# Kernel tuning notes

Measured on AMD Instinct MI355X. Metric: run time of the kernel, lower is better.

The kernel has to match this reference:

```python
import jax, jax.numpy as jnp
import numpy as np

NUM_HEADS = 8


def setup_inputs() -> dict:
    key = jax.random.key(0)
    ks = jax.random.split(key, 9)
    B, S, E = 16, 2048, 768
    s = 0.02
    return {
        "features": jax.random.normal(ks[0], (B, S, E), jnp.float32),
        "in_proj_w": jax.random.normal(ks[1], (3 * E, E), jnp.float32) * s,
        "in_proj_b": jnp.zeros((3 * E,), jnp.float32),
        "out_proj_w": jax.random.normal(ks[2], (E, E), jnp.float32) * s,
        "out_proj_b": jnp.zeros((E,), jnp.float32),
        "w1": jax.random.normal(ks[3], (384, E), jnp.float32) * s,
        "b1": jnp.zeros((384,), jnp.float32),
        "w2": jax.random.normal(ks[4], (1, 384), jnp.float32) * s,
        "b2": jnp.zeros((1,), jnp.float32),
    }


def reference(features, in_proj_w, in_proj_b, out_proj_w, out_proj_b, w1, b1, w2, b2):
    # torch nn.MultiheadAttention default batch_first=False: dim 0 is the
    # attended sequence axis (length B here), dim 1 is the MHA batch (S).
    B, S, E = features.shape
    H = NUM_HEADS
    Dh = E // H
    qkv = features @ in_proj_w.T + in_proj_b          # (B, S, 3E)
    q, k, v = jnp.split(qkv, 3, axis=-1)
    q = q.reshape(B, S, H, Dh)
    k = k.reshape(B, S, H, Dh)
    v = v.reshape(B, S, H, Dh)
    scale = 1.0 / jnp.sqrt(jnp.asarray(Dh, features.dtype))
    # attention over axis-0 positions (l, m in 0..B-1), per (s, h)
    scores = jnp.einsum('lshd,mshd->shlm', q * scale, k)
    attn = jax.nn.softmax(scores, axis=-1)
    ctx = jnp.einsum('shlm,mshd->lshd', attn, v).reshape(B, S, E)
    attn_out = ctx @ out_proj_w.T + out_proj_b        # (B, S, E)
    # batched 2-layer MLP (replaces the Python per-row loop)
    h = jax.nn.relu(attn_out @ w1.T + b1)             # (B, S, 384)
    prob = h @ w2.T + b2                              # (B, S, 1)
    contacts = jnp.broadcast_to(prob, (B, S, S))      # contacts[:, i, :] = prob[:, i]
    return contacts
```

## Files before the change

### kernel.cpp

```cpp
#include <hip/hip_runtime.h>

typedef unsigned short u16;
typedef __attribute__((ext_vector_type(8))) __bf16 bf16x8;
typedef __attribute__((ext_vector_type(4))) float floatx4;

#define B_DIM  16
#define S_DIM  2048
#define E_DIM  768
#define HEADS  8
#define DHEAD  96
#define MROWS  32768
#define QKV_LD 2304
#define NT     12

#define GLDS(gp, lp) __builtin_amdgcn_global_load_lds( \
    (const __attribute__((address_space(1))) void*)(gp), \
    (__attribute__((address_space(3))) void*)(lp), 16, 0, 0)

__device__ __forceinline__ u16 f2b(float f) {
    unsigned u = __float_as_uint(f);
    u += 0x7fffu + ((u >> 16) & 1u);
    return (u16)(u >> 16);
}
__device__ __forceinline__ float blo(unsigned u) { return __uint_as_float(u << 16); }
__device__ __forceinline__ float bhi(unsigned u) { return __uint_as_float(u & 0xffff0000u); }

__device__ __forceinline__ void axpy8(float* acc, float p, uint4 v) {
    acc[0] += p * blo(v.x); acc[1] += p * bhi(v.x);
    acc[2] += p * blo(v.y); acc[3] += p * bhi(v.y);
    acc[4] += p * blo(v.z); acc[5] += p * bhi(v.z);
    acc[6] += p * blo(v.w); acc[7] += p * bhi(v.w);
}

__device__ __forceinline__ bf16x8 ldsw(const u16* half_base, int rowh, int cb) {
    return *(const bf16x8*)((const char*)half_base + rowh * 128 + (cb ^ ((rowh & 7) << 4)));
}

#define PB0 24576
#define PB1 26304
#define PB2 26592
#define PB3 27168
#define PB4 27552
__global__ __launch_bounds__(256) void prep(const float* __restrict__ features,
                                            const float* __restrict__ in_proj_w,
                                            const float* __restrict__ w1,
                                            const float* __restrict__ out_proj_w,
                                            const float* __restrict__ bo,
                                            const float* __restrict__ b1,
                                            u16* __restrict__ fbf, u16* __restrict__ wib,
                                            u16* __restrict__ w1b, u16* __restrict__ WoT,
                                            float* __restrict__ cbuf) {
    __shared__ float tsh[32][33];
    const int b = blockIdx.x, tid = threadIdx.x;
    if (b < PB2) {
        const float* src; u16* dst; long i;
        if (b < PB0)      { src = features;  dst = fbf; i = (long)b * 256 + tid; }
        else if (b < PB1) { src = in_proj_w; dst = wib; i = (long)(b - PB0) * 256 + tid; }
        else              { src = w1;        dst = w1b; i = (long)(b - PB1) * 256 + tid; }
        float4 f = ((const float4*)src)[i];
        ushort4 r;
        r.x = f2b(f.x); r.y = f2b(f.y); r.z = f2b(f.z); r.w = f2b(f.w);
        ((ushort4*)dst)[i] = r;
    } else if (b < PB3) {
        const int t = b - PB2;
        const int bxT = t % 24, byT = t / 24;
        const int tx = tid & 31, ty = tid >> 5;
        int x = bxT * 32 + tx;
        int y = byT * 32 + ty;
#pragma unroll
        for (int j = 0; j < 4; j++) tsh[ty + j * 8][tx] = out_proj_w[(long)(y + j * 8) * 768 + x];
        __syncthreads();
        x = byT * 32 + tx;
        y = bxT * 32 + ty;
#pragma unroll
        for (int j = 0; j < 4; j++) WoT[(long)(y + j * 8) * 768 + x] = f2b(tsh[tx][ty + j * 8]);
    } else {
        const int n = b - PB3;
        const float* row = w1 + (long)n * 768;
        float s = row[tid] * bo[tid] + row[tid + 256] * bo[tid + 256] + row[tid + 512] * bo[tid + 512];
#pragma unroll
        for (int off = 32; off > 0; off >>= 1) s += __shfl_xor(s, off);
        if ((tid & 63) == 0) tsh[0][tid >> 6] = s;
        __syncthreads();
        if (tid == 0) cbuf[n] = tsh[0][0] + tsh[0][1] + tsh[0][2] + tsh[0][3] + b1[n];
    }
}

__global__ __launch_bounds__(512, 2) void qkv256(const u16* __restrict__ A,
                                                 const u16* __restrict__ W,
                                                 const float* __restrict__ bias,
                                                 u16* __restrict__ Cout,
                                                 const u16* __restrict__ gA,
                                                 const u16* __restrict__ gW,
                                                 u16* __restrict__ gC) {
    __shared__ __align__(16) u16 lds[2 * 32768];
    const int tid = threadIdx.x;
    const int bx  = blockIdx.x;
    int bm, bn, ldc, Mvalid; const u16 *Aa, *Ww; const float* bs; u16* Co; bool perm;
    if (bx < 1152) {
        const int xcd = bx & 7;
        const int q   = bx >> 3;
        bn = q % 9;
        bm = (q / 9) * 8 + xcd;
        Aa = A; Ww = W; bs = bias; Co = Cout; ldc = QKV_LD; perm = true; Mvalid = 1 << 30;
    } else {
        const int g = bx - 1152;
        bn = g % 3; bm = g / 3;
        Aa = gA; Ww = gW; bs = nullptr; Co = gC; ldc = 768; perm = false; Mvalid = 384;
    }
    const int r0 = tid >> 3,        r1 = (tid + 512) >> 3;
    const int q0 = (tid & 7) ^ (r0 & 7), q1 = ((tid + 512) & 7) ^ (r1 & 7);
    const u16* pA0 = Aa + (long)(bm * 256 + r0) * 768 + q0 * 8;
    const u16* pA1 = Aa + (long)(bm * 256 + r1) * 768 + q1 * 8;
    const u16* pB0 = Ww + (long)(bn * 256 + r0) * 768 + q0 * 8;
    const u16* pB1 = Ww + (long)(bn * 256 + r1) * 768 + q1 * 8;
    u16* dA0 = lds + tid * 8;
    u16* dA1 = lds + 4096 + tid * 8;
    u16* dB0 = lds + 16384 + tid * 8;
    u16* dB1 = lds + 16384 + 4096 + tid * 8;

#define IS_A(h, p, t) do { \
    GLDS(pA0 + (h) * 98304 + (t) * 64, dA0 + (p) * 32768 + (h) * 8192); \
    GLDS(pA1 + (h) * 98304 + (t) * 64, dA1 + (p) * 32768 + (h) * 8192); } while (0)
#define IS_B(h, p, t) do { \
    GLDS(pB0 + (h) * 98304 + (t) * 64, dB0 + (p) * 32768 + (h) * 8192); \
    GLDS(pB1 + (h) * 98304 + (t) * 64, dB1 + (p) * 32768 + (h) * 8192); } while (0)
#define MFMA_PRE() do { \
    __builtin_amdgcn_s_barrier(); \
    asm volatile("s_waitcnt lgkmcnt(0)" ::: "memory"); \
    __builtin_amdgcn_sched_barrier(0); \
    __builtin_amdgcn_s_setprio(1); } while (0)
#define MFMA_POST() do { \
    __builtin_amdgcn_s_setprio(0); \
    __builtin_amdgcn_s_barrier(); } while (0)

    const int lane = tid & 63, wid = tid >> 6;
    const int wr = wid >> 2, wc = wid & 3;
    const int fr = lane & 15, fg = lane >> 4;
    const int fq2 = fg * 16;
    const int wb  = (wc & 1) * 64;
    const u16* bufA_base = lds + wr * 8192;
    const u16* bufB_base = lds + 16384 + (wc >> 1) * 8192;

    IS_A(0, 0, 0); IS_A(1, 0, 0); IS_B(0, 0, 0); IS_B(1, 0, 0);
    IS_A(0, 1, 1); IS_A(1, 1, 1);
    asm volatile("s_waitcnt vmcnt(4)" ::: "memory");
    __builtin_amdgcn_s_barrier();

    floatx4 acc[8][4] = {};
#pragma unroll 2
    for (int t = 0; t < NT; ++t) {
        const int p = t & 1, pn = p ^ 1;
        const u16* bA = bufA_base + p * 32768;
        const u16* bB = bufB_base + p * 32768;
        bf16x8 aF[4], bF[4];
#pragma unroll
        for (int i = 0; i < 4; ++i) aF[i] = ldsw(bA, i * 16 + fr, fq2);
#pragma unroll
        for (int j = 0; j < 4; ++j) bF[j] = ldsw(bB, wb + j * 16 + fr, fq2);
        if (t + 1 < NT) IS_B(0, pn, t + 1);
        MFMA_PRE();
#pragma unroll
        for (int i = 0; i < 4; ++i)
#pragma unroll
            for (int j = 0; j < 4; ++j)
                acc[i][j] = __builtin_amdgcn_mfma_f32_16x16x32_bf16(aF[i], bF[j], acc[i][j], 0, 0, 0);
        MFMA_POST();
#pragma unroll
        for (int i = 0; i < 4; ++i) aF[i] = ldsw(bA, (i + 4) * 16 + fr, fq2);
        if (t + 1 < NT) IS_B(1, pn, t + 1);
        MFMA_PRE();
#pragma unroll
        for (int i = 0; i < 4; ++i)
#pragma unroll
            for (int j = 0; j < 4; ++j)
                acc[i + 4][j] = __builtin_amdgcn_mfma_f32_16x16x32_bf16(aF[i], bF[j], acc[i + 4][j], 0, 0, 0);
        MFMA_POST();
#pragma unroll
        for (int i = 0; i < 4; ++i) aF[i] = ldsw(bA, i * 16 + fr, 64 + fq2);
#pragma unroll
        for (int j = 0; j < 4; ++j) bF[j] = ldsw(bB, wb + j * 16 + fr, 64 + fq2);
        MFMA_PRE();
#pragma unroll
        for (int i = 0; i < 4; ++i)
#pragma unroll
            for (int j = 0; j < 4; ++j)
                acc[i][j] = __builtin_amdgcn_mfma_f32_16x16x32_bf16(aF[i], bF[j], acc[i][j], 0, 0, 0);
        MFMA_POST();
#pragma unroll
        for (int i = 0; i < 4; ++i) aF[i] = ldsw(bA, (i + 4) * 16 + fr, 64 + fq2);
        MFMA_PRE();
#pragma unroll
        for (int i = 0; i < 4; ++i)
#pragma unroll
            for (int j = 0; j < 4; ++j)
                acc[i + 4][j] = __builtin_amdgcn_mfma_f32_16x16x32_bf16(aF[i], bF[j], acc[i + 4][j], 0, 0, 0);
        MFMA_POST();
        if (t + 2 < NT) {
            IS_A(0, p, t + 2); IS_A(1, p, t + 2);
            asm volatile("s_waitcnt vmcnt(4)" ::: "memory");
            __builtin_amdgcn_s_barrier();
        } else if (t + 1 < NT) {
            asm volatile("s_waitcnt vmcnt(0)" ::: "memory");
            __builtin_amdgcn_s_barrier();
        }
    }

    const int rq = fg * 4;
    float bvj[4];
#pragma unroll
    for (int j = 0; j < 4; ++j) bvj[j] = bs ? bs[bn * 256 + wc * 64 + j * 16 + fr] : 0.f;
    u16* strip = lds + wid * 2304;
    const int sr = lane >> 3, sc = lane & 7;
#pragma unroll
    for (int pass = 0; pass < 4; ++pass) {
#pragma unroll
        for (int ii = 0; ii < 2; ++ii) {
            const int i = pass * 2 + ii;
#pragma unroll
            for (int j = 0; j < 4; ++j)
#pragma unroll
                for (int r = 0; r < 4; ++r)
                    strip[(ii * 16 + rq + r) * 72 + j * 16 + fr] = f2b(acc[i][j][r] + bvj[j]);
        }
#pragma unroll
        for (int it = 0; it < 4; ++it) {
            const int lr = it * 8 + sr;
            uint4 v = *(const uint4*)(strip + lr * 72 + sc * 8);
            const int rl = bm * 256 + wr * 128 + pass * 32 + lr;
            if (rl < Mvalid) {
                const long grow = perm ? (long)(((rl & 2047) << 4) | (rl >> 11)) : (long)rl;
                *(uint4*)(Co + grow * ldc + bn * 256 + wc * 64 + sc * 8) = v;
            }
        }
    }
#undef IS_A
#undef IS_B
#undef MFMA_PRE
#undef MFMA_POST
}

__global__ __launch_bounds__(256) void attn_kernel(u16* __restrict__ qkv) {
    __shared__ __align__(16) u16 sQKV[3 * 16 * 384];
    __shared__ float sS[4][16][16];
    const int tid = threadIdx.x;
    const int bx  = blockIdx.x;
    const int xcd   = bx & 7;
    const int hh    = (bx >> 3) & 1;
    const int inner = bx >> 4;
    const int s = (xcd << 8) | inner;
    const u16* base = qkv + (long)s * 16 * QKV_LD + hh * 384;

#pragma unroll
    for (int it = 0; it < 9; it++) {
        const int id = it * 256 + tid;
        const int t = id / 768, within = id % 768;
        const int l = within / 48, c = within % 48;
        const int csrc = c ^ (l & 7);
        GLDS(base + (long)l * QKV_LD + t * E_DIM + csrc * 8, sQKV + id * 8);
    }
    __syncthreads();

    const int lane = tid & 63;
    const int w    = tid >> 6;
    const int fr   = lane & 15;
    const int fg   = lane >> 4;
    floatx4 acc = {};
#pragma unroll
    for (int st = 0; st < 3; st++) {
        const int ch  = w * 12 + st * 4 + fg;
        const int chs = ch ^ (fr & 7);
        bf16x8 qa = *(const bf16x8*)(sQKV + fr * 384 + chs * 8);
        bf16x8 kb = *(const bf16x8*)(sQKV + 6144 + fr * 384 + chs * 8);
        acc = __builtin_amdgcn_mfma_f32_16x16x32_bf16(qa, kb, acc, 0, 0, 0);
    }
    const int rq = fg * 4;
#pragma unroll
    for (int r = 0; r < 4; r++) {
        float sc = acc[r] * 0.10206207261596577f;
        float mx = sc;
#pragma unroll
        for (int off = 8; off > 0; off >>= 1) mx = fmaxf(mx, __shfl_xor(mx, off));
        float e = __expf(sc - mx);
        float sum = e;
#pragma unroll
        for (int off = 8; off > 0; off >>= 1) sum += __shfl_xor(sum, off);
        sS[w][rq + r][fr] = e / sum;
    }
    __syncthreads();

#pragma unroll
    for (int j = 0; j < 3; j++) {
        const int task = j * 256 + tid;
        const int h = task / 192, rem = task % 192, ll = rem / 12, c = rem % 12;
        float a[8] = {};
#pragma unroll
        for (int mm = 0; mm < 16; mm++) {
            const float p = sS[h][ll][mm];
            const int ch = (h * 12 + c) ^ (mm & 7);
            uint4 vw = *(const uint4*)(sQKV + 12288 + mm * 384 + ch * 8);
            axpy8(a, p, vw);
        }
        uint4 o;
        o.x = (unsigned)f2b(a[0]) | ((unsigned)f2b(a[1]) << 16);
        o.y = (unsigned)f2b(a[2]) | ((unsigned)f2b(a[3]) << 16);
        o.z = (unsigned)f2b(a[4]) | ((unsigned)f2b(a[5]) << 16);
        o.w = (unsigned)f2b(a[6]) | ((unsigned)f2b(a[7]) << 16);
        *(uint4*)(qkv + ((long)s * 16 + ll) * QKV_LD + (hh * 4 + h) * DHEAD + c * 8) = o;
    }
}

__global__ __launch_bounds__(256) void mlp_gemm(const u16* __restrict__ A, int lda,
                                                const u16* __restrict__ G,
                                                const float* __restrict__ cbias,
                                                const float* __restrict__ w2,
                                                float* __restrict__ part) {
    __shared__ __align__(16) u16 sA[2 * 128 * 32];
    __shared__ __align__(16) u16 sB[2 * 128 * 32];
    __shared__ float rowsum[128];
    const int tid = threadIdx.x;
    const int bx  = blockIdx.x;
    const int xcd = bx & 7;
    const int q   = bx >> 3;
    const int bn  = q % 3;
    const int t   = q / 3;
    const int bm  = (xcd << 5) | t;
    if (tid < 128) rowsum[tid] = 0.f;
    const int lane = tid & 63;
    const int wid  = tid >> 6;
    const int wm   = (wid >> 1) * 64;
    const int wn   = (wid & 1) * 64;
    const int ar = tid >> 2;
    const int ac = (tid & 3) * 8;
    const u16* Ap = A + (long)(bm * 128 + ar) * lda + ac;
    const u16* Wp = G + (long)(bn * 128 + ar) * 768 + ac;
    const long a2 = (long)64 * lda;
    const long w2s = (long)64 * 768;
    const int fr = lane & 15;
    const int fq = (lane >> 4) * 8;
    const int rq = (lane >> 4) * 4;

    floatx4 acc[4][4] = {};
    for (int k0 = 0; k0 < 768; k0 += 64) {
#pragma unroll
        for (int h = 0; h < 2; h++) {
            GLDS(Ap + k0 + h * 32,       sA + h * 4096 + tid * 8);
            GLDS(Ap + a2 + k0 + h * 32,  sA + h * 4096 + 2048 + tid * 8);
            GLDS(Wp + k0 + h * 32,       sB + h * 4096 + tid * 8);
            GLDS(Wp + w2s + k0 + h * 32, sB + h * 4096 + 2048 + tid * 8);
        }
        __syncthreads();
#pragma unroll
        for (int h = 0; h < 2; h++) {
            bf16x8 aF[4], bF[4];
#pragma unroll
            for (int i = 0; i < 4; i++) {
                aF[i] = *(const bf16x8*)(sA + h * 4096 + (wm + i * 16 + fr) * 32 + fq);
                bF[i] = *(const bf16x8*)(sB + h * 4096 + (wn + i * 16 + fr) * 32 + fq);
            }
#pragma unroll
            for (int i = 0; i < 4; i++)
#pragma unroll
                for (int j = 0; j < 4; j++)
                    acc[i][j] = __builtin_amdgcn_mfma_f32_16x16x32_bf16(aF[i], bF[j], acc[i][j], 0, 0, 0);
        }
        __syncthreads();
    }
    float partl[4][4] = {};
#pragma unroll
    for (int j = 0; j < 4; j++) {
        const int col = bn * 128 + wn + j * 16 + fr;
        const float cv = cbias[col];
        const float wv = w2[col];
#pragma unroll
        for (int i = 0; i < 4; i++)
#pragma unroll
            for (int r = 0; r < 4; r++)
                partl[i][r] += fmaxf(acc[i][j][r] + cv, 0.f) * wv;
    }
#pragma unroll
    for (int i = 0; i < 4; i++)
#pragma unroll
        for (int r = 0; r < 4; r++) {
            float v = partl[i][r];
#pragma unroll
            for (int off = 8; off > 0; off >>= 1) v += __shfl_xor(v, off);
            if (fr == 0) atomicAdd(&rowsum[wm + i * 16 + rq + r], v);
        }
    __syncthreads();
    if (tid < 128) part[(long)bn * MROWS + bm * 128 + tid] = rowsum[tid];
}

__global__ __launch_bounds__(256) void bcast_kernel(const float* __restrict__ part,
                                                    const float* __restrict__ b2,
                                                    float* __restrict__ out) {
    const int tid = threadIdx.x;
    const long s  = blockIdx.x;
    const float b2v = b2[0];
#pragma unroll
    for (int l = 0; l < 16; l++) {
        const long p = s * 16 + l;
        const float pv = part[p] + part[MROWS + p] + part[2 * MROWS + p] + b2v;
        floatx4 v4 = {pv, pv, pv, pv};
        floatx4* dst = (floatx4*)(out + ((long)l * S_DIM + s) * S_DIM);
        __builtin_nontemporal_store(v4, dst + tid);
        __builtin_nontemporal_store(v4, dst + tid + 256);
    }
}

extern "C" void kernel_launch(void* const* d_in, const int* in_sizes, int n_in,
                              void* d_out, int out_size, void* d_ws, size_t ws_size,
                              hipStream_t stream) {
    const float* features   = (const float*)d_in[0];
    const float* in_proj_b  = (const float*)d_in[2];
    const float* out_proj_b = (const float*)d_in[4];
    const float* b1 = (const float*)d_in[6];
    const float* w2 = (const float*)d_in[7];
    const float* b2 = (const float*)d_in[8];
    float* out = (float*)d_out;

    char* p = (char*)d_ws;
    u16* fbf = (u16*)p; p += (size_t)MROWS * E_DIM * 2;
    u16* wib = (u16*)p; p += (size_t)QKV_LD * E_DIM * 2;
    u16* w1b = (u16*)p; p += (size_t)384 * E_DIM * 2;
    u16* WoT = (u16*)p; p += (size_t)E_DIM * E_DIM * 2;
    u16* Gbf = (u16*)p; p += (size_t)384 * E_DIM * 2;
    float* cbuf  = (float*)p; p += 384 * 4;
    float* partb = (float*)p; p += (size_t)3 * MROWS * 4;
    p = (char*)(((size_t)p + 255) & ~(size_t)255);
    u16* qkv = (u16*)p; p += (size_t)MROWS * QKV_LD * 2;
    u16* ctx = qkv;

    prep<<<PB4, 256, 0, stream>>>(features, (const float*)d_in[1], (const float*)d_in[5],
                                  (const float*)d_in[3], out_proj_b, b1,
                                  fbf, wib, w1b, WoT, cbuf);
    qkv256<<<1158, 512, 0, stream>>>(fbf, wib, in_proj_b, qkv, w1b, WoT, Gbf);
    attn_kernel<<<S_DIM * 2, 256, 0, stream>>>(qkv);
    mlp_gemm<<<768, 256, 0, stream>>>(ctx, QKV_LD, Gbf, cbuf, w2, partb);
    bcast_kernel<<<S_DIM, 256, 0, stream>>>(partb, b2, out);
}
```

Measured before the change: 552.1 us.

## Use MFMA for attention P·V with split-bf16 probabilities; schedule small GEMM blocks first

Replaces the scalar FMA loop for the attention-times-V product with a bf16 MFMA. The probabilities are split into hi and lo bf16 parts so precision is kept, the V column fragments are gathered from unswizzled LDS, and the context is staged in LDS for coalesced 16-byte stores. It also moves the small auxiliary GEMM tiles to the front of the qkv256 grid so they no longer form a tail. In exchange, the V column gather uses scalar 2-byte LDS reads, and the extra LDS round trip adds a sync.

```diff
diff --git a/kernel.cpp b/kernel.cpp
--- a/kernel.cpp
+++ b/kernel.cpp
@@ -23,14 +23,6 @@
     return (u16)(u >> 16);
 }
 __device__ __forceinline__ float blo(unsigned u) { return __uint_as_float(u << 16); }
-__device__ __forceinline__ float bhi(unsigned u) { return __uint_as_float(u & 0xffff0000u); }
-
-__device__ __forceinline__ void axpy8(float* acc, float p, uint4 v) {
-    acc[0] += p * blo(v.x); acc[1] += p * bhi(v.x);
-    acc[2] += p * blo(v.y); acc[3] += p * bhi(v.y);
-    acc[4] += p * blo(v.z); acc[5] += p * bhi(v.z);
-    acc[6] += p * blo(v.w); acc[7] += p * bhi(v.w);
-}
 
 __device__ __forceinline__ bf16x8 ldsw(const u16* half_base, int rowh, int cb) {
     return *(const bf16x8*)((const char*)half_base + rowh * 128 + (cb ^ ((rowh & 7) << 4)));
@@ -97,16 +89,15 @@
     const int tid = threadIdx.x;
     const int bx  = blockIdx.x;
     int bm, bn, ldc, Mvalid; const u16 *Aa, *Ww; const float* bs; u16* Co; bool perm;
-    if (bx < 1152) {
+    if (bx < 6) {
+        bn = bx % 3; bm = bx / 3;
+        Aa = gA; Ww = gW; bs = nullptr; Co = gC; ldc = 768; perm = false; Mvalid = 384;
+    } else {
         const int xcd = bx & 7;
-        const int q   = bx >> 3;
+        const int q   = (bx >> 3) - ((bx & 7) < 6 ? 1 : 0);
         bn = q % 9;
         bm = (q / 9) * 8 + xcd;
         Aa = A; Ww = W; bs = bias; Co = Cout; ldc = QKV_LD; perm = true; Mvalid = 1 << 30;
-    } else {
-        const int g = bx - 1152;
-        bn = g % 3; bm = g / 3;
-        Aa = gA; Ww = gW; bs = nullptr; Co = gC; ldc = 768; perm = false; Mvalid = 384;
     }
     const int r0 = tid >> 3,        r1 = (tid + 512) >> 3;
     const int q0 = (tid & 7) ^ (r0 & 7), q1 = ((tid + 512) & 7) ^ (r1 & 7);
@@ -242,7 +233,7 @@
 
 __global__ __launch_bounds__(256) void attn_kernel(u16* __restrict__ qkv) {
     __shared__ __align__(16) u16 sQKV[3 * 16 * 384];
-    __shared__ float sS[4][16][16];
+    __shared__ __align__(16) u16 sP[4][2][16][16];
     const int tid = threadIdx.x;
     const int bx  = blockIdx.x;
     const int xcd   = bx & 7;
@@ -256,7 +247,7 @@
         const int id = it * 256 + tid;
         const int t = id / 768, within = id % 768;
         const int l = within / 48, c = within % 48;
-        const int csrc = c ^ (l & 7);
+        const int csrc = (t < 2) ? (c ^ (l & 7)) : c;
         GLDS(base + (long)l * QKV_LD + t * E_DIM + csrc * 8, sQKV + id * 8);
     }
     __syncthreads();
@@ -285,28 +276,40 @@
         float sum = e;
 #pragma unroll
         for (int off = 8; off > 0; off >>= 1) sum += __shfl_xor(sum, off);
-        sS[w][rq + r][fr] = e / sum;
+        const float pv = e / sum;
+        const u16 phi = f2b(pv);
+        const u16 plo = f2b(pv - blo((unsigned)phi));
+        sP[w][0][rq + r][fr] = phi;
+        sP[w][1][rq + r][fr] = plo;
+    }
+    __syncthreads();
+
+    const bf16x8 pfrag = *(const bf16x8*)(&sP[w][fg >> 1][fr][(fg & 1) * 8]);
+    const int mbase = (fg & 1) * 8;
+    u16* ctx = sQKV;
+#pragma unroll
+    for (int dt = 0; dt < 6; dt++) {
+        const int d = w * 96 + dt * 16 + fr;
+        const u16* vcol = sQKV + 12288 + mbase * 384 + d;
+        unsigned vv0 = vcol[0 * 384], vv1 = vcol[1 * 384], vv2 = vcol[2 * 384], vv3 = vcol[3 * 384];
+        unsigned vv4 = vcol[4 * 384], vv5 = vcol[5 * 384], vv6 = vcol[6 * 384], vv7 = vcol[7 * 384];
+        unsigned pk0 = vv0 | (vv1 << 16), pk1 = vv2 | (vv3 << 16);
+        unsigned pk2 = vv4 | (vv5 << 16), pk3 = vv6 | (vv7 << 16);
+        uint4 pkv = {pk0, pk1, pk2, pk3};
+        bf16x8 bfrag = *(const bf16x8*)&pkv;
+        floatx4 o = {};
+        o = __builtin_amdgcn_mfma_f32_16x16x32_bf16(pfrag, bfrag, o, 0, 0, 0);
+#pragma unroll
+        for (int r = 0; r < 4; r++) ctx[(rq + r) * 384 + d] = f2b(o[r]);
     }
     __syncthreads();
 
 #pragma unroll
     for (int j = 0; j < 3; j++) {
         const int task = j * 256 + tid;
-        const int h = task / 192, rem = task % 192, ll = rem / 12, c = rem % 12;
-        float a[8] = {};
-#pragma unroll
-        for (int mm = 0; mm < 16; mm++) {
-            const float p = sS[h][ll][mm];
-            const int ch = (h * 12 + c) ^ (mm & 7);
-            uint4 vw = *(const uint4*)(sQKV + 12288 + mm * 384 + ch * 8);
-            axpy8(a, p, vw);
-        }
-        uint4 o;
-        o.x = (unsigned)f2b(a[0]) | ((unsigned)f2b(a[1]) << 16);
-        o.y = (unsigned)f2b(a[2]) | ((unsigned)f2b(a[3]) << 16);
-        o.z = (unsigned)f2b(a[4]) | ((unsigned)f2b(a[5]) << 16);
-        o.w = (unsigned)f2b(a[6]) | ((unsigned)f2b(a[7]) << 16);
-        *(uint4*)(qkv + ((long)s * 16 + ll) * QKV_LD + (hh * 4 + h) * DHEAD + c * 8) = o;
+        const int l = task / 48, c = task % 48;
+        uint4 v = *(const uint4*)(sQKV + l * 384 + c * 8);
+        *(uint4*)(qkv + ((long)s * 16 + l) * QKV_LD + hh * 384 + c * 8) = v;
     }
 }
 
```

After: 548.6 us. About the same (-0.6%).
